# Kernel tuning notes

Hardware: AMD Instinct MI355X
Metric: run time of the kernel (lower is better)

## Reference

```python
import jax, jax.numpy as jnp
import numpy as np

N_QUBITS = 16
DEPTH = 4
BATCH = 512

# Convention: wire 0 is the most-significant bit of the state index (PennyLane default).

def _rx(t):
    # t: scalar or (B,) real angle -> (2,2) or (B,2,2) complex RX matrix
    h = 0.5 * t
    c = jnp.cos(h).astype(jnp.complex64)
    s = (-1j * jnp.sin(h)).astype(jnp.complex64)
    return jnp.stack([jnp.stack([c, s], -1), jnp.stack([s, c], -1)], -2)

def _ry(t):
    h = 0.5 * t
    c = jnp.cos(h).astype(jnp.complex64)
    s = jnp.sin(h).astype(jnp.complex64)
    return jnp.stack([jnp.stack([c, -s], -1), jnp.stack([s, c], -1)], -2)

def _rz(t):
    e = jnp.exp(-0.5j * t.astype(jnp.complex64))  # diag(e^{-it/2}, e^{+it/2})
    z = jnp.zeros_like(e)
    return jnp.stack([jnp.stack([e, z], -1), jnp.stack([z, jnp.conj(e)], -1)], -2)

def _apply_1q(state, U, q, n):
    # state: (B, 2^n); U: (2,2) shared or (B,2,2) per-batch
    B = state.shape[0]
    L, R = 2 ** q, 2 ** (n - q - 1)
    s = state.reshape(B, L, 2, R)
    if U.ndim == 2:
        s = jnp.einsum('ij,bljr->blir', U, s)
    else:
        s = jnp.einsum('bij,bljr->blir', U, s)
    return s.reshape(B, -1)

def _apply_cnot(state, c, t, n):
    # flips target bit t where control bit c == 1
    B = state.shape[0]
    a, b = min(c, t), max(c, t)
    s = state.reshape(B, 2 ** a, 2, 2 ** (b - a - 1), 2, 2 ** (n - b - 1))
    if c < t:
        # control axis=2, target axis=4
        s1 = s[:, :, 1]                      # (B, 2^a, mid, 2, rest)
        flipped = s1[:, :, :, ::-1, :]
        s = jnp.stack([s[:, :, 0], flipped], axis=2)
    else:
        # control axis=4, target axis=2
        s1 = s[:, :, :, :, 1, :]             # (B, 2^a, 2, mid, rest)
        flipped = s1[:, :, ::-1]
        s = jnp.stack([s[:, :, :, :, 0, :], flipped], axis=4)
    return s.reshape(B, -1)

def _circuit(x, params):
    B, n = x.shape
    depth = params.shape[0]
    state = jnp.zeros((B, 2 ** n), jnp.complex64).at[:, 0].set(1.0)
    # data encoding: batched RX per wire
    for i in range(n):
        state = _apply_1q(state, _rx(x[:, i]), i, n)
    for layer in range(depth):
        for i in range(n):
            # circuit applies RZ then RX then RY -> fuse into one 2x2 matrix
            U = _ry(params[layer, i, 2]) @ _rx(params[layer, i, 1]) @ _rz(params[layer, i, 0])
            state = _apply_1q(state, U, i, n)
        for i in range(n - 1):
            state = _apply_cnot(state, i, i + 1, n)
        state = _apply_cnot(state, n - 1, 0, n)
    # <Z_i> = P(bit_i = 0) - P(bit_i = 1)
    probs = state.real ** 2 + state.imag ** 2
    expz = []
    for i in range(n):
        p = probs.reshape(B, 2 ** i, 2, 2 ** (n - i - 1))
        expz.append(p[:, :, 0].sum((1, 2)) - p[:, :, 1].sum((1, 2)))
    return jnp.stack(expz, axis=1)  # (B, n_qubits)


def setup_inputs() -> dict:
    key = jax.random.key(0)
    k1, k2 = jax.random.split(key)
    x = jax.random.normal(k1, (BATCH, N_QUBITS), dtype=jnp.float32)
    params = jax.random.normal(k2, (DEPTH, N_QUBITS, 3), dtype=jnp.float32)
    return {"x": x, "params": params}


def reference(x, params):
    return _circuit(x, params)
```

## Files before the change

### kernel.cpp

```cpp
#include <hip/hip_runtime.h>


#define NQ 16
#define TPB 256

typedef float __attribute__((ext_vector_type(2))) f2;

__device__ __forceinline__ f2 f2s(float s) { return (f2){s, s}; }

__device__ __forceinline__ f2 cmulpk(f2 a, f2 b) {
    f2 bs = { -b.y, b.x };
    f2 r = f2s(a.x) * b;
    return __builtin_elementwise_fma(f2s(a.y), bs, r);
}

__device__ __forceinline__ void computeU(const float* params, int layer, int q, f2* U) {
    const float* p = params + (layer*NQ + q)*3;
    float s0, c0, s1, c1, s2, c2;
    sincosf(0.5f*p[0], &s0, &c0);
    sincosf(0.5f*p[1], &s1, &c1);
    sincosf(0.5f*p[2], &s2, &c2);
    f2 m00 = { c1*c0, -c1*s0};
    f2 m01 = { s1*s0, -s1*c0};
    f2 m10 = {-s1*s0, -s1*c0};
    f2 m11 = { c1*c0,  c1*s0};
    U[0] = c2*m00 - s2*m10;
    U[1] = c2*m01 - s2*m11;
    U[2] = s2*m00 + c2*m10;
    U[3] = s2*m01 + c2*m11;
}

template<int MASK>
__device__ __forceinline__ void gate32(f2* A, f2 u00, f2 u01, f2 u10, f2 u11) {
    #pragma unroll
    for (int a = 0; a < 32; ++a) {
        if (!(a & MASK)) {
            f2 x = A[a], y = A[a | MASK];
            f2 xs = { -x.y, x.x };
            f2 ys = { -y.y, y.x };
            f2 nx = f2s(u00.x) * x;
            nx = __builtin_elementwise_fma(f2s(u00.y), xs, nx);
            nx = __builtin_elementwise_fma(f2s(u01.x), y,  nx);
            nx = __builtin_elementwise_fma(f2s(u01.y), ys, nx);
            f2 ny = f2s(u10.x) * x;
            ny = __builtin_elementwise_fma(f2s(u10.y), xs, ny);
            ny = __builtin_elementwise_fma(f2s(u11.x), y,  ny);
            ny = __builtin_elementwise_fma(f2s(u11.y), ys, ny);
            A[a] = nx; A[a | MASK] = ny;
        }
    }
}

__device__ __forceinline__ constexpr int permB(int ad) {
    return (ad & 1)
         | ((((ad >> 1) ^ (ad >> 2)) & 1) << 1)
         | ((((ad >> 2) ^ (ad >> 3)) & 1) << 2)
         | ((((ad >> 3) ^ (ad >> 4)) & 1) << 3)
         | ((((ad >> 4) ^  ad      ) & 1) << 4);
}

__device__ __forceinline__ int b_qb(int tt) { return (tt < 3) ? (15 - tt) : (14 - tt); }

__global__ __launch_bounds__(TPB, 4) void qc_B1_gen(
    const float* __restrict__ x, const float* __restrict__ params,
    f2* __restrict__ st)
{
    __shared__ __align__(16) f2 S[4096];
    __shared__ f2 Ush[11][4];
    __shared__ f2 V[16][2];

    const int t    = threadIdx.x;
    const int b    = blockIdx.x >> 3;
    const int fixb = blockIdx.x & 7;
    f2* base = st + ((size_t)b << NQ);

    if (t < 16) {
        f2 U[4];
        computeU(params, 0, t, U);
        float s, c;
        sincosf(0.5f * x[b*NQ + t], &s, &c);
        V[15 - t][0] = (f2){U[0].x*c + U[1].y*s, U[0].y*c - U[1].x*s};
        V[15 - t][1] = (f2){U[2].x*c + U[3].y*s, U[2].y*c - U[3].x*s};
    } else if (t < 27) {
        int tt = t - 16;
        computeU(params, 1, b_qb(tt), Ush[tt]);
    }
    __syncthreads();

    const int f0 = fixb & 1, f1 = (fixb >> 1) & 1, f2b = (fixb >> 2) & 1;
    const int t0 = t & 1,  t7 = (t >> 7) & 1;

    f2 pre = V[4][(t ^ (t >> 1)) & 1];
    #pragma unroll
    for (int bb = 5; bb <= 10; ++bb)
        pre = cmulpk(pre, V[bb][((t >> (bb - 4)) ^ (t >> (bb - 3))) & 1]);
    pre = cmulpk(pre, V[11][t7 ^ f0]);
    pre = cmulpk(pre, V[12][f0 ^ f1]);
    pre = cmulpk(pre, V[13][f1 ^ f2b]);

    f2 P0 = cmulpk(pre, V[3][t0]);
    f2 P1 = cmulpk(pre, V[3][1 ^ t0]);
    f2 Q[4];
    Q[0] = cmulpk(P0, V[2][0]); Q[1] = cmulpk(P1, V[2][0]);
    Q[2] = cmulpk(P0, V[2][1]); Q[3] = cmulpk(P1, V[2][1]);
    f2 Rr[4];
    Rr[0] = cmulpk(V[0][0], V[1][0]); Rr[1] = cmulpk(V[0][1], V[1][0]);
    Rr[2] = cmulpk(V[0][0], V[1][1]); Rr[3] = cmulpk(V[0][1], V[1][1]);
    f2 G0 = cmulpk(V[15][0], V[14][f2b]);
    f2 G1 = cmulpk(V[15][1], V[14][1 ^ f2b]);
    f2 TT[8];
    #pragma unroll
    for (int e = 0; e < 4; ++e) {
        TT[2*e]     = cmulpk(G0, Rr[e]);
        TT[2*e + 1] = cmulpk(G1, Rr[e]);
    }

    f2 A[32];
    #pragma unroll
    for (int a = 0; a < 32; ++a) {
        const int a0 = a & 1;
        const int e1 = ((a >> 1) ^ (a >> 2)) & 1;
        const int e2 = ((a >> 2) ^ (a >> 3)) & 1;
        const int e3 = ((a >> 3) ^ (a >> 4)) & 1;
        const int e4 = ((a >> 4) ^  a      ) & 1;
        A[a] = cmulpk(Q[a0 + 2*e4], TT[e1 + 2*e2 + 4*e3]);
    }

    gate32<4> (A, Ush[0][0], Ush[0][1], Ush[0][2], Ush[0][3]);
    gate32<8> (A, Ush[1][0], Ush[1][1], Ush[1][2], Ush[1][3]);
    gate32<16>(A, Ush[2][0], Ush[2][1], Ush[2][2], Ush[2][3]);

    #pragma unroll
    for (int h = 0; h < 2; ++h) {
        __syncthreads();
        #pragma unroll
        for (int c = 0; c < 8; ++c) {
            int slot = ((t << 1) | (c << 9)) ^ (((t >> 4) & 7) << 1);
            f2 a0 = A[h*16 + 2*c], a1 = A[h*16 + 2*c + 1];
            *(float4*)&S[slot] = make_float4(a0.x, a0.y, a1.x, a1.y);
        }
        __syncthreads();
        #pragma unroll
        for (int rr = 0; rr < 16; ++rr) {
            int jj = (t & 1) | (rr << 1) | (((t >> 1) & 15) << 5) | (((t >> 5) & 7) << 9);
            A[h*16 + rr] = S[jj ^ (((t >> 1) & 7) << 1)];
        }
    }

    gate32<1>(A, Ush[3][0], Ush[3][1], Ush[3][2], Ush[3][3]);
    gate32<2>(A, Ush[4][0], Ush[4][1], Ush[4][2], Ush[4][3]);
    gate32<4>(A, Ush[5][0], Ush[5][1], Ush[5][2], Ush[5][3]);
    gate32<8>(A, Ush[6][0], Ush[6][1], Ush[6][2], Ush[6][3]);

    #pragma unroll
    for (int h = 0; h < 2; ++h) {
        __syncthreads();
        #pragma unroll
        for (int rr = 0; rr < 16; ++rr) {
            int jj = (t & 1) | (rr << 1) | (((t >> 1) & 15) << 5) | (((t >> 5) & 7) << 9);
            S[jj ^ (((t >> 1) & 7) << 1)] = A[h*16 + rr];
        }
        __syncthreads();
        #pragma unroll
        for (int rr = 0; rr < 16; ++rr) {
            int jj = (t & 31) | (rr << 5) | (((t >> 5) & 7) << 9);
            A[h*16 + rr] = S[jj ^ ((rr & 7) << 1)];
        }
    }

    gate32<1>(A, Ush[7][0],  Ush[7][1],  Ush[7][2],  Ush[7][3]);
    gate32<2>(A, Ush[8][0],  Ush[8][1],  Ush[8][2],  Ush[8][3]);
    gate32<4>(A, Ush[9][0],  Ush[9][1],  Ush[9][2],  Ush[9][3]);
    gate32<8>(A, Ush[10][0], Ush[10][1], Ush[10][2], Ush[10][3]);

    #pragma unroll
    for (int h = 0; h < 2; ++h) {
        #pragma unroll
        for (int rr = 0; rr < 16; ++rr) {
            int d = (t & 31) | (rr << 5) | (((t >> 5) & 7) << 9) | (h << 12);
            int m = (d & 511) | (fixb << 9) | (((d >> 9) & 1) << 12) | ((d >> 10) << 13);
            base[m] = A[h*16 + rr];
        }
    }
}

__global__ __launch_bounds__(TPB, 4) void qc_B_heavy(
    const float* __restrict__ params, f2* __restrict__ st, int lm)
{
    __shared__ __align__(16) f2 S[4096];
    __shared__ f2 Ush[11][4];

    const int t    = threadIdx.x;
    const int b    = blockIdx.x >> 3;
    const int fixb = blockIdx.x & 7;
    f2* base = st + ((size_t)b << NQ);

    if (t < 11) computeU(params, lm, b_qb(t), Ush[t]);

    f2 R[32];
    #pragma unroll
    for (int k = 0; k < 16; ++k) {
        int j = 2*(t + 256*k);
        int m = (j & 511) | (fixb << 9) | (((j >> 9) & 1) << 12) | ((j >> 10) << 13);
        float4 v = *(const float4*)(base + m);
        R[2*k]   = (f2){v.x, v.y};
        R[2*k+1] = (f2){v.z, v.w};
    }
    f2 A[32];
    #pragma unroll
    for (int a = 0; a < 32; ++a) A[a] = R[permB(a)];
    __syncthreads();

    gate32<4> (A, Ush[0][0], Ush[0][1], Ush[0][2], Ush[0][3]);
    gate32<8> (A, Ush[1][0], Ush[1][1], Ush[1][2], Ush[1][3]);
    gate32<16>(A, Ush[2][0], Ush[2][1], Ush[2][2], Ush[2][3]);

    #pragma unroll
    for (int h = 0; h < 2; ++h) {
        __syncthreads();
        #pragma unroll
        for (int c = 0; c < 8; ++c) {
            int slot = ((t << 1) | (c << 9)) ^ (((t >> 4) & 7) << 1);
            f2 a0 = A[h*16 + 2*c], a1 = A[h*16 + 2*c + 1];
            *(float4*)&S[slot] = make_float4(a0.x, a0.y, a1.x, a1.y);
        }
        __syncthreads();
        #pragma unroll
        for (int rr = 0; rr < 16; ++rr) {
            int jj = (t & 1) | (rr << 1) | (((t >> 1) & 15) << 5) | (((t >> 5) & 7) << 9);
            A[h*16 + rr] = S[jj ^ (((t >> 1) & 7) << 1)];
        }
    }

    gate32<1>(A, Ush[3][0], Ush[3][1], Ush[3][2], Ush[3][3]);
    gate32<2>(A, Ush[4][0], Ush[4][1], Ush[4][2], Ush[4][3]);
    gate32<4>(A, Ush[5][0], Ush[5][1], Ush[5][2], Ush[5][3]);
    gate32<8>(A, Ush[6][0], Ush[6][1], Ush[6][2], Ush[6][3]);

    #pragma unroll
    for (int h = 0; h < 2; ++h) {
        __syncthreads();
        #pragma unroll
        for (int rr = 0; rr < 16; ++rr) {
            int jj = (t & 1) | (rr << 1) | (((t >> 1) & 15) << 5) | (((t >> 5) & 7) << 9);
            S[jj ^ (((t >> 1) & 7) << 1)] = A[h*16 + rr];
        }
        __syncthreads();
        #pragma unroll
        for (int rr = 0; rr < 16; ++rr) {
            int jj = (t & 31) | (rr << 5) | (((t >> 5) & 7) << 9);
            A[h*16 + rr] = S[jj ^ ((rr & 7) << 1)];
        }
    }

    gate32<1>(A, Ush[7][0],  Ush[7][1],  Ush[7][2],  Ush[7][3]);
    gate32<2>(A, Ush[8][0],  Ush[8][1],  Ush[8][2],  Ush[8][3]);
    gate32<4>(A, Ush[9][0],  Ush[9][1],  Ush[9][2],  Ush[9][3]);
    gate32<8>(A, Ush[10][0], Ush[10][1], Ush[10][2], Ush[10][3]);

    #pragma unroll
    for (int h = 0; h < 2; ++h) {
        #pragma unroll
        for (int rr = 0; rr < 16; ++rr) {
            int d = (t & 31) | (rr << 5) | (((t >> 5) & 7) << 9) | (h << 12);
            int m = (d & 511) | (fixb << 9) | (((d >> 9) & 1) << 12) | ((d >> 10) << 13);
            base[m] = A[h*16 + rr];
        }
    }
}

__global__ __launch_bounds__(TPB, 4) void qc_A_lite(
    const float* __restrict__ params, f2* __restrict__ st, int layer)
{
    __shared__ __align__(16) f2 S[4096];
    __shared__ f2 Ush[5][4];
    const int t    = threadIdx.x;
    const int b    = blockIdx.x >> 3;
    const int fix3 = blockIdx.x & 7;
    f2* base = st + ((size_t)b << NQ) + (fix3 << 13);

    if (t < 5) computeU(params, layer, (t == 0) ? 12 : 4 - t, Ush[t]);

    f2 A[32];
    const float4* src = (const float4*)base;
    #pragma unroll
    for (int k = 0; k < 16; ++k) {
        float4 v = src[t + 256*k];
        A[2*k]   = (f2){v.x, v.y};
        A[2*k+1] = (f2){v.z, v.w};
    }
    __syncthreads();

    gate32<1> (A, Ush[0][0], Ush[0][1], Ush[0][2], Ush[0][3]);
    gate32<2> (A, Ush[1][0], Ush[1][1], Ush[1][2], Ush[1][3]);
    gate32<4> (A, Ush[2][0], Ush[2][1], Ush[2][2], Ush[2][3]);
    gate32<8> (A, Ush[3][0], Ush[3][1], Ush[3][2], Ush[3][3]);
    gate32<16>(A, Ush[4][0], Ush[4][1], Ush[4][2], Ush[4][3]);

    float4* dst = (float4*)base;
    #pragma unroll
    for (int h = 0; h < 2; ++h) {
        __syncthreads();
        #pragma unroll
        for (int c = 0; c < 8; ++c) {
            int slot = ((t << 1) | (c << 9)) ^ (((t >> 4) & 7) << 1);
            f2 a0 = A[h*16 + 2*c], a1 = A[h*16 + 2*c + 1];
            *(float4*)&S[slot] = make_float4(a0.x, a0.y, a1.x, a1.y);
        }
        __syncthreads();
        #pragma unroll
        for (int k = 0; k < 8; ++k) {
            int d  = 2*(t + 256*k);
            int i0 = d ^ (d >> 1) ^ (h << 11);
            int i1 = (d+1) ^ ((d+1) >> 1) ^ (h << 11);
            f2 a0 = S[i0 ^ (((i0 >> 5) & 7) << 1)];
            f2 a1 = S[i1 ^ (((i1 >> 5) & 7) << 1)];
            dst[(t + 256*k) | (h << 11)] = make_float4(a0.x, a0.y, a1.x, a1.y);
        }
    }
}

__global__ __launch_bounds__(TPB) void qc_A_final(
    const float* __restrict__ params, const f2* __restrict__ st,
    float* __restrict__ out)
{
    __shared__ f2 Ush[5][4];
    __shared__ float F[16*272];
    const int t    = threadIdx.x;
    const int b    = blockIdx.x >> 3;
    const int fix3 = blockIdx.x & 7;
    const f2* base = st + ((size_t)b << NQ) + (fix3 << 13);

    if (t < 5) computeU(params, 3, (t == 0) ? 12 : 4 - t, Ush[t]);

    f2 A[32];
    const float4* src = (const float4*)base;
    #pragma unroll
    for (int k = 0; k < 16; ++k) {
        float4 v = src[t + 256*k];
        A[2*k]   = (f2){v.x, v.y};
        A[2*k+1] = (f2){v.z, v.w};
    }
    __syncthreads();

    gate32<1> (A, Ush[0][0], Ush[0][1], Ush[0][2], Ush[0][3]);
    gate32<2> (A, Ush[1][0], Ush[1][1], Ush[1][2], Ush[1][3]);
    gate32<4> (A, Ush[2][0], Ush[2][1], Ush[2][2], Ush[2][3]);
    gate32<8> (A, Ush[3][0], Ush[3][1], Ush[3][2], Ush[3][3]);
    gate32<16>(A, Ush[4][0], Ush[4][1], Ush[4][2], Ush[4][3]);

    float m1 = 0.f, m2 = 0.f, m3 = 0.f, m4 = 0.f, m5 = 0.f;
    #pragma unroll
    for (int a = 0; a < 32; ++a) {
        float p = A[a].x*A[a].x + A[a].y*A[a].y;
        m1 += (__popc(a & 0x1E) & 1) ? -p : p;
        m2 += (__popc(a & 0x1F) & 1) ? -p : p;
        m3 += (__popc(a & 0x1C) & 1) ? -p : p;
        m4 += (__popc(a & 0x18) & 1) ? -p : p;
        m5 += (__popc(a & 0x0F) & 1) ? -p : p;
    }
    const int pt = __popc(t) & 1;
    const int pf = __popc(fix3) & 1;
    float acc[NQ];
    acc[0] = ((pt ^ pf) & 1) ? -m5 : m5;
    acc[1] = m4;
    acc[2] = m3;
    acc[3] = m1;
    #pragma unroll
    for (int q = 4; q <= 11; ++q) {
        int s = __popc(t >> (11 - q)) & 1;
        acc[q] = s ? -m1 : m1;
    }
    acc[12] = pt ? -m2 : m2;
    acc[13] = ((pt ^ (fix3 >> 2)) & 1) ? -m2 : m2;
    acc[14] = ((pt ^ __popc(fix3 >> 1)) & 1) ? -m2 : m2;
    acc[15] = ((pt ^ pf) & 1) ? -m2 : m2;

    #pragma unroll
    for (int q = 0; q < NQ; ++q) F[q*272 + t] = acc[q];
    __syncthreads();
    const int qq = t >> 4, ii = t & 15;
    float s = 0.f;
    #pragma unroll
    for (int c = 0; c < 16; ++c) s += F[qq*272 + ii + 16*c];
    s += __shfl_down(s, 8, 16);
    s += __shfl_down(s, 4, 16);
    s += __shfl_down(s, 2, 16);
    s += __shfl_down(s, 1, 16);
    if (ii == 0) atomicAdd(&out[b*NQ + qq], s);
}

extern "C" void kernel_launch(void* const* d_in, const int* in_sizes, int n_in,
                              void* d_out, int out_size, void* d_ws, size_t ws_size,
                              hipStream_t stream)
{
    (void)in_sizes; (void)n_in; (void)ws_size;
    const float* x      = (const float*)d_in[0];
    const float* params = (const float*)d_in[1];
    float* out = (float*)d_out;
    f2* st = (f2*)d_ws;

    hipMemsetAsync(d_out, 0, (size_t)out_size * sizeof(float), stream);
    qc_B1_gen <<<dim3(512*8), dim3(TPB), 0, stream>>>(x, params, st);
    qc_A_lite <<<dim3(512*8), dim3(TPB), 0, stream>>>(params, st, 1);
    qc_B_heavy<<<dim3(512*8), dim3(TPB), 0, stream>>>(params, st, 2);
    qc_A_lite <<<dim3(512*8), dim3(TPB), 0, stream>>>(params, st, 2);
    qc_B_heavy<<<dim3(512*8), dim3(TPB), 0, stream>>>(params, st, 3);
    qc_A_final<<<dim3(512*8), dim3(TPB), 0, stream>>>(params, st, out);
}
```

Measured before the change: 555.1 us.

## Rebalance gate stages between B and A kernels, moving four qubits' gates to A side

New measurement: 558.9 us. About the same (+0.7%).

```diff
diff --git a/kernel.cpp b/kernel.cpp
--- a/kernel.cpp
+++ b/kernel.cpp
@@ -59,14 +59,72 @@
          | ((((ad >> 4) ^  ad      ) & 1) << 4);
 }
 
-__device__ __forceinline__ int b_qb(int tt) { return (tt < 3) ? (15 - tt) : (14 - tt); }
+__device__ __forceinline__ void transpose_1to3(f2* A, f2* S, int t) {
+    #pragma unroll
+    for (int h = 0; h < 2; ++h) {
+        __syncthreads();
+        #pragma unroll
+        for (int c = 0; c < 8; ++c) {
+            int slot = ((t << 1) | (c << 9)) ^ (((t >> 4) & 7) << 1);
+            f2 a0 = A[h*16 + 2*c], a1 = A[h*16 + 2*c + 1];
+            *(float4*)&S[slot] = make_float4(a0.x, a0.y, a1.x, a1.y);
+        }
+        __syncthreads();
+        #pragma unroll
+        for (int rr = 0; rr < 16; ++rr) {
+            int jj = (t & 31) | (rr << 5) | (((t >> 5) & 7) << 9);
+            A[h*16 + rr] = S[jj ^ ((rr & 7) << 1)];
+        }
+    }
+}
+
+__device__ __forceinline__ void transpose_1to2(f2* A, f2* S, int t) {
+    #pragma unroll
+    for (int h = 0; h < 2; ++h) {
+        __syncthreads();
+        #pragma unroll
+        for (int c = 0; c < 8; ++c) {
+            int slot = ((t << 1) | (c << 9)) ^ (((t >> 4) & 7) << 1);
+            f2 a0 = A[h*16 + 2*c], a1 = A[h*16 + 2*c + 1];
+            *(float4*)&S[slot] = make_float4(a0.x, a0.y, a1.x, a1.y);
+        }
+        __syncthreads();
+        #pragma unroll
+        for (int rr = 0; rr < 16; ++rr) {
+            int jj = (t & 1) | (rr << 1) | (((t >> 1) & 15) << 5) | (((t >> 5) & 7) << 9);
+            A[h*16 + rr] = S[jj ^ (((t >> 1) & 7) << 1)];
+        }
+    }
+}
+
+__device__ __forceinline__ void b_tail_gates_store(
+    f2* A, f2* S, const f2 (*Ush)[4], int t, int fixb, f2* base)
+{
+    transpose_1to3(A, S, t);
+    gate32<1>(A, Ush[3][0], Ush[3][1], Ush[3][2], Ush[3][3]);
+    gate32<2>(A, Ush[4][0], Ush[4][1], Ush[4][2], Ush[4][3]);
+    gate32<4>(A, Ush[5][0], Ush[5][1], Ush[5][2], Ush[5][3]);
+    gate32<8>(A, Ush[6][0], Ush[6][1], Ush[6][2], Ush[6][3]);
+    #pragma unroll
+    for (int h = 0; h < 2; ++h) {
+        #pragma unroll
+        for (int rr = 0; rr < 16; ++rr) {
+            int d = (t & 31) | (rr << 5) | (((t >> 5) & 7) << 9) | (h << 12);
+            int m = (d & 511) | (fixb << 9) | (((d >> 9) & 1) << 12) | ((d >> 10) << 13);
+            base[m] = A[h*16 + rr];
+        }
+    }
+}
+
+__device__ __forceinline__ int b_qb(int tt) { return (tt < 3) ? (15 - tt) : (10 - tt); }
+__device__ __forceinline__ int a_qb(int tt) { return (tt == 0) ? 12 : (tt < 5) ? (4 - tt) : (16 - tt); }
 
 __global__ __launch_bounds__(TPB, 4) void qc_B1_gen(
     const float* __restrict__ x, const float* __restrict__ params,
     f2* __restrict__ st)
 {
     __shared__ __align__(16) f2 S[4096];
-    __shared__ f2 Ush[11][4];
+    __shared__ f2 Ush[7][4];
     __shared__ f2 V[16][2];
 
     const int t    = threadIdx.x;
@@ -81,7 +139,7 @@
         sincosf(0.5f * x[b*NQ + t], &s, &c);
         V[15 - t][0] = (f2){U[0].x*c + U[1].y*s, U[0].y*c - U[1].x*s};
         V[15 - t][1] = (f2){U[2].x*c + U[3].y*s, U[2].y*c - U[3].x*s};
-    } else if (t < 27) {
+    } else if (t < 23) {
         int tt = t - 16;
         computeU(params, 1, b_qb(tt), Ush[tt]);
     }
@@ -130,72 +188,21 @@
     gate32<8> (A, Ush[1][0], Ush[1][1], Ush[1][2], Ush[1][3]);
     gate32<16>(A, Ush[2][0], Ush[2][1], Ush[2][2], Ush[2][3]);
 
-    #pragma unroll
-    for (int h = 0; h < 2; ++h) {
-        __syncthreads();
-        #pragma unroll
-        for (int c = 0; c < 8; ++c) {
-            int slot = ((t << 1) | (c << 9)) ^ (((t >> 4) & 7) << 1);
-            f2 a0 = A[h*16 + 2*c], a1 = A[h*16 + 2*c + 1];
-            *(float4*)&S[slot] = make_float4(a0.x, a0.y, a1.x, a1.y);
-        }
-        __syncthreads();
-        #pragma unroll
-        for (int rr = 0; rr < 16; ++rr) {
-            int jj = (t & 1) | (rr << 1) | (((t >> 1) & 15) << 5) | (((t >> 5) & 7) << 9);
-            A[h*16 + rr] = S[jj ^ (((t >> 1) & 7) << 1)];
-        }
-    }
-
-    gate32<1>(A, Ush[3][0], Ush[3][1], Ush[3][2], Ush[3][3]);
-    gate32<2>(A, Ush[4][0], Ush[4][1], Ush[4][2], Ush[4][3]);
-    gate32<4>(A, Ush[5][0], Ush[5][1], Ush[5][2], Ush[5][3]);
-    gate32<8>(A, Ush[6][0], Ush[6][1], Ush[6][2], Ush[6][3]);
-
-    #pragma unroll
-    for (int h = 0; h < 2; ++h) {
-        __syncthreads();
-        #pragma unroll
-        for (int rr = 0; rr < 16; ++rr) {
-            int jj = (t & 1) | (rr << 1) | (((t >> 1) & 15) << 5) | (((t >> 5) & 7) << 9);
-            S[jj ^ (((t >> 1) & 7) << 1)] = A[h*16 + rr];
-        }
-        __syncthreads();
-        #pragma unroll
-        for (int rr = 0; rr < 16; ++rr) {
-            int jj = (t & 31) | (rr << 5) | (((t >> 5) & 7) << 9);
-            A[h*16 + rr] = S[jj ^ ((rr & 7) << 1)];
-        }
-    }
-
-    gate32<1>(A, Ush[7][0],  Ush[7][1],  Ush[7][2],  Ush[7][3]);
-    gate32<2>(A, Ush[8][0],  Ush[8][1],  Ush[8][2],  Ush[8][3]);
-    gate32<4>(A, Ush[9][0],  Ush[9][1],  Ush[9][2],  Ush[9][3]);
-    gate32<8>(A, Ush[10][0], Ush[10][1], Ush[10][2], Ush[10][3]);
-
-    #pragma unroll
-    for (int h = 0; h < 2; ++h) {
-        #pragma unroll
-        for (int rr = 0; rr < 16; ++rr) {
-            int d = (t & 31) | (rr << 5) | (((t >> 5) & 7) << 9) | (h << 12);
-            int m = (d & 511) | (fixb << 9) | (((d >> 9) & 1) << 12) | ((d >> 10) << 13);
-            base[m] = A[h*16 + rr];
-        }
-    }
+    b_tail_gates_store(A, S, Ush, t, fixb, base);
 }
 
 __global__ __launch_bounds__(TPB, 4) void qc_B_heavy(
     const float* __restrict__ params, f2* __restrict__ st, int lm)
 {
     __shared__ __align__(16) f2 S[4096];
-    __shared__ f2 Ush[11][4];
+    __shared__ f2 Ush[7][4];
 
     const int t    = threadIdx.x;
     const int b    = blockIdx.x >> 3;
     const int fixb = blockIdx.x & 7;
     f2* base = st + ((size_t)b << NQ);
 
-    if (t < 11) computeU(params, lm, b_qb(t), Ush[t]);
+    if (t < 7) computeU(params, lm, b_qb(t), Ush[t]);
 
     f2 R[32];
     #pragma unroll
@@ -215,71 +222,20 @@
     gate32<8> (A, Ush[1][0], Ush[1][1], Ush[1][2], Ush[1][3]);
     gate32<16>(A, Ush[2][0], Ush[2][1], Ush[2][2], Ush[2][3]);
 
-    #pragma unroll
-    for (int h = 0; h < 2; ++h) {
-        __syncthreads();
-        #pragma unroll
-        for (int c = 0; c < 8; ++c) {
-            int slot = ((t << 1) | (c << 9)) ^ (((t >> 4) & 7) << 1);
-            f2 a0 = A[h*16 + 2*c], a1 = A[h*16 + 2*c + 1];
-            *(float4*)&S[slot] = make_float4(a0.x, a0.y, a1.x, a1.y);
-        }
-        __syncthreads();
-        #pragma unroll
-        for (int rr = 0; rr < 16; ++rr) {
-            int jj = (t & 1) | (rr << 1) | (((t >> 1) & 15) << 5) | (((t >> 5) & 7) << 9);
-            A[h*16 + rr] = S[jj ^ (((t >> 1) & 7) << 1)];
-        }
-    }
-
-    gate32<1>(A, Ush[3][0], Ush[3][1], Ush[3][2], Ush[3][3]);
-    gate32<2>(A, Ush[4][0], Ush[4][1], Ush[4][2], Ush[4][3]);
-    gate32<4>(A, Ush[5][0], Ush[5][1], Ush[5][2], Ush[5][3]);
-    gate32<8>(A, Ush[6][0], Ush[6][1], Ush[6][2], Ush[6][3]);
-
-    #pragma unroll
-    for (int h = 0; h < 2; ++h) {
-        __syncthreads();
-        #pragma unroll
-        for (int rr = 0; rr < 16; ++rr) {
-            int jj = (t & 1) | (rr << 1) | (((t >> 1) & 15) << 5) | (((t >> 5) & 7) << 9);
-            S[jj ^ (((t >> 1) & 7) << 1)] = A[h*16 + rr];
-        }
-        __syncthreads();
-        #pragma unroll
-        for (int rr = 0; rr < 16; ++rr) {
-            int jj = (t & 31) | (rr << 5) | (((t >> 5) & 7) << 9);
-            A[h*16 + rr] = S[jj ^ ((rr & 7) << 1)];
-        }
-    }
-
-    gate32<1>(A, Ush[7][0],  Ush[7][1],  Ush[7][2],  Ush[7][3]);
-    gate32<2>(A, Ush[8][0],  Ush[8][1],  Ush[8][2],  Ush[8][3]);
-    gate32<4>(A, Ush[9][0],  Ush[9][1],  Ush[9][2],  Ush[9][3]);
-    gate32<8>(A, Ush[10][0], Ush[10][1], Ush[10][2], Ush[10][3]);
-
-    #pragma unroll
-    for (int h = 0; h < 2; ++h) {
-        #pragma unroll
-        for (int rr = 0; rr < 16; ++rr) {
-            int d = (t & 31) | (rr << 5) | (((t >> 5) & 7) << 9) | (h << 12);
-            int m = (d & 511) | (fixb << 9) | (((d >> 9) & 1) << 12) | ((d >> 10) << 13);
-            base[m] = A[h*16 + rr];
-        }
-    }
+    b_tail_gates_store(A, S, Ush, t, fixb, base);
 }
 
 __global__ __launch_bounds__(TPB, 4) void qc_A_lite(
     const float* __restrict__ params, f2* __restrict__ st, int layer)
 {
     __shared__ __align__(16) f2 S[4096];
-    __shared__ f2 Ush[5][4];
+    __shared__ f2 Ush[9][4];
     const int t    = threadIdx.x;
     const int b    = blockIdx.x >> 3;
     const int fix3 = blockIdx.x & 7;
     f2* base = st + ((size_t)b << NQ) + (fix3 << 13);
 
-    if (t < 5) computeU(params, layer, (t == 0) ? 12 : 4 - t, Ush[t]);
+    if (t < 9) computeU(params, layer, a_qb(t), Ush[t]);
 
     f2 A[32];
     const float4* src = (const float4*)base;
@@ -297,15 +253,20 @@
     gate32<8> (A, Ush[3][0], Ush[3][1], Ush[3][2], Ush[3][3]);
     gate32<16>(A, Ush[4][0], Ush[4][1], Ush[4][2], Ush[4][3]);
 
+    transpose_1to2(A, S, t);
+    gate32<1>(A, Ush[5][0], Ush[5][1], Ush[5][2], Ush[5][3]);
+    gate32<2>(A, Ush[6][0], Ush[6][1], Ush[6][2], Ush[6][3]);
+    gate32<4>(A, Ush[7][0], Ush[7][1], Ush[7][2], Ush[7][3]);
+    gate32<8>(A, Ush[8][0], Ush[8][1], Ush[8][2], Ush[8][3]);
+
     float4* dst = (float4*)base;
     #pragma unroll
     for (int h = 0; h < 2; ++h) {
         __syncthreads();
         #pragma unroll
-        for (int c = 0; c < 8; ++c) {
-            int slot = ((t << 1) | (c << 9)) ^ (((t >> 4) & 7) << 1);
-            f2 a0 = A[h*16 + 2*c], a1 = A[h*16 + 2*c + 1];
-            *(float4*)&S[slot] = make_float4(a0.x, a0.y, a1.x, a1.y);
+        for (int rr = 0; rr < 16; ++rr) {
+            int jj = (t & 1) | (rr << 1) | (((t >> 1) & 15) << 5) | (((t >> 5) & 7) << 9);
+            S[jj ^ (((t >> 1) & 7) << 1)] = A[h*16 + rr];
         }
         __syncthreads();
         #pragma unroll
@@ -320,18 +281,19 @@
     }
 }
 
-__global__ __launch_bounds__(TPB) void qc_A_final(
+__global__ __launch_bounds__(TPB, 4) void qc_A_final(
     const float* __restrict__ params, const f2* __restrict__ st,
     float* __restrict__ out)
 {
-    __shared__ f2 Ush[5][4];
-    __shared__ float F[16*272];
+    __shared__ __align__(16) f2 S[4096];
+    __shared__ f2 Ush[9][4];
+    float* F = (float*)S;
     const int t    = threadIdx.x;
     const int b    = blockIdx.x >> 3;
     const int fix3 = blockIdx.x & 7;
     const f2* base = st + ((size_t)b << NQ) + (fix3 << 13);
 
-    if (t < 5) computeU(params, 3, (t == 0) ? 12 : 4 - t, Ush[t]);
+    if (t < 9) computeU(params, 3, a_qb(t), Ush[t]);
 
     f2 A[32];
     const float4* src = (const float4*)base;
@@ -349,33 +311,51 @@
     gate32<8> (A, Ush[3][0], Ush[3][1], Ush[3][2], Ush[3][3]);
     gate32<16>(A, Ush[4][0], Ush[4][1], Ush[4][2], Ush[4][3]);
 
-    float m1 = 0.f, m2 = 0.f, m3 = 0.f, m4 = 0.f, m5 = 0.f;
-    #pragma unroll
-    for (int a = 0; a < 32; ++a) {
-        float p = A[a].x*A[a].x + A[a].y*A[a].y;
-        m1 += (__popc(a & 0x1E) & 1) ? -p : p;
-        m2 += (__popc(a & 0x1F) & 1) ? -p : p;
-        m3 += (__popc(a & 0x1C) & 1) ? -p : p;
-        m4 += (__popc(a & 0x18) & 1) ? -p : p;
-        m5 += (__popc(a & 0x0F) & 1) ? -p : p;
-    }
-    const int pt = __popc(t) & 1;
-    const int pf = __popc(fix3) & 1;
+    transpose_1to2(A, S, t);
+    gate32<1>(A, Ush[5][0], Ush[5][1], Ush[5][2], Ush[5][3]);
+    gate32<2>(A, Ush[6][0], Ush[6][1], Ush[6][2], Ush[6][3]);
+    gate32<4>(A, Ush[7][0], Ush[7][1], Ush[7][2], Ush[7][3]);
+    gate32<8>(A, Ush[8][0], Ush[8][1], Ush[8][2], Ush[8][3]);
+
+    float B1 = 0.f, B2 = 0.f, B3 = 0.f, B4 = 0.f, B5 = 0.f, B6 = 0.f;
+    #pragma unroll
+    for (int h = 0; h < 2; ++h) {
+        #pragma unroll
+        for (int rr = 0; rr < 16; ++rr) {
+            f2 v = A[h*16 + rr];
+            float p = v.x*v.x + v.y*v.y;
+            int pr = __popc(rr);
+            B1 += ((pr ^ h) & 1)              ? -p : p;
+            B2 += ((__popc(rr >> 1) ^ h) & 1) ? -p : p;
+            B3 += ((__popc(rr >> 2) ^ h) & 1) ? -p : p;
+            B4 += (((rr >> 3) ^ h) & 1)       ? -p : p;
+            B5 += h                           ? -p : p;
+            B6 += (pr & 1)                    ? -p : p;
+        }
+    }
+
+    const int pt  = __popc(t) & 1;
+    const int pt1 = __popc(t >> 1) & 1;
+    const int pf  = __popc(fix3) & 1;
     float acc[NQ];
-    acc[0] = ((pt ^ pf) & 1) ? -m5 : m5;
-    acc[1] = m4;
-    acc[2] = m3;
-    acc[3] = m1;
-    #pragma unroll
-    for (int q = 4; q <= 11; ++q) {
-        int s = __popc(t >> (11 - q)) & 1;
-        acc[q] = s ? -m1 : m1;
-    }
-    acc[12] = pt ? -m2 : m2;
-    acc[13] = ((pt ^ (fix3 >> 2)) & 1) ? -m2 : m2;
-    acc[14] = ((pt ^ __popc(fix3 >> 1)) & 1) ? -m2 : m2;
-    acc[15] = ((pt ^ pf) & 1) ? -m2 : m2;
-
+    acc[0]  = ((pf ^ pt) & 1)                  ? -B6 : B6;
+    acc[1]  = ((t >> 7) & 1)                   ? -B5 : B5;
+    acc[2]  = (__popc(t >> 6) & 1)             ? -B5 : B5;
+    acc[3]  = (__popc(t >> 5) & 1)             ? -B5 : B5;
+    acc[4]  = (__popc(t >> 4) & 1)             ? -B5 : B5;
+    acc[5]  = (__popc(t >> 3) & 1)             ? -B5 : B5;
+    acc[6]  = (__popc(t >> 2) & 1)             ? -B5 : B5;
+    acc[7]  = pt1                              ? -B5 : B5;
+    acc[8]  = pt1                              ? -B4 : B4;
+    acc[9]  = pt1                              ? -B3 : B3;
+    acc[10] = pt1                              ? -B2 : B2;
+    acc[11] = pt1                              ? -B1 : B1;
+    acc[12] = pt                               ? -B1 : B1;
+    acc[13] = ((((fix3 >> 2) & 1) ^ pt) & 1)   ? -B1 : B1;
+    acc[14] = ((__popc(fix3 >> 1) ^ pt) & 1)   ? -B1 : B1;
+    acc[15] = ((pf ^ pt) & 1)                  ? -B1 : B1;
+
+    __syncthreads();
     #pragma unroll
     for (int q = 0; q < NQ; ++q) F[q*272 + t] = acc[q];
     __syncthreads();
```
